# Kernel optimization log

Measured on AMD Instinct MI355X. Metric: run time of the kernel, lower is better.

## Reference

```python
import jax, jax.numpy as jnp
import numpy as np

E, D, H, K = 640000, 128, 64, 8  # edges, edge-feat dim, hidden=max(32, D//2), n_experts
TEMPERATURE = 1.0


def setup_inputs() -> dict:
    key = jax.random.key(0)
    ks = jax.random.split(key, 6)
    u = lambda k, shape, fan: jax.random.uniform(k, shape, jnp.float32, -1.0 / np.sqrt(fan), 1.0 / np.sqrt(fan))
    return {
        "edge_features": jax.random.normal(ks[0], (E, D), jnp.float32),
        "w1": u(ks[1], (D, H), D),
        "b1": u(ks[2], (H,), D),
        "w2": u(ks[3], (H, K), H),
        "b2": u(ks[4], (K,), H),
        "w_proj": u(ks[5], (D, K), D),
    }


def reference(edge_features, w1, b1, w2, b2, w_proj):
    # edge MLP router: [E, D] -> [E, H] -> [E, K]
    h = jax.nn.relu(edge_features @ w1 + b1)
    logits = (h @ w2 + b2) / TEMPERATURE
    # soft gating
    alpha = jax.nn.softmax(logits, axis=-1)  # [E, K]
    # expert scores (no bias) and weighted reduce
    expert_scores = edge_features @ w_proj   # [E, K]
    fused_edge = jnp.sum(alpha * expert_scores, axis=-1)  # [E]
    return fused_edge, alpha
```

## Files before the change

kernel.cpp:

```cpp
#include <hip/hip_runtime.h>
#include <hip/hip_bf16.h>

typedef __bf16 bf16x8 __attribute__((ext_vector_type(8)));
typedef float  f32x4  __attribute__((ext_vector_type(4)));

#define MFMA(a, b, c) __builtin_amdgcn_mfma_f32_16x16x32_bf16((a), (b), (c), 0, 0, 0)


__device__ __forceinline__ int swz(int row, int byteInRow) {
    return row * 256 + (byteInRow ^ ((row & 7) << 4));
}

__global__ __launch_bounds__(256, 3) void edge_moe_kernel(
    const float* __restrict__ x,  const float* __restrict__ w1,
    const float* __restrict__ b1, const float* __restrict__ w2,
    const float* __restrict__ b2, const float* __restrict__ wp,
    float* __restrict__ outFused, float* __restrict__ outAlpha, int E)
{
    __shared__ __align__(16) char lds[49152];
    char* XH = lds;
    char* XL = lds + 16384;
    char* HF = lds + 32768;

    const int tid  = threadIdx.x;
    const int lane = tid & 63;
    const int wid  = tid >> 6;
    const int lc   = lane & 15;
    const int lg   = lane >> 4;

    bf16x8 w1h[4], w1l[4], w2h[2], w2l[2], wph[4], wpl[4];
#pragma unroll
    for (int kk = 0; kk < 4; ++kk) {
        bf16x8 h, l;
#pragma unroll
        for (int j = 0; j < 8; ++j) {
            int kidx = kk * 32 + lg * 8 + j;
            float v = w1[kidx * 64 + wid * 16 + lc];
            __bf16 hb = (__bf16)v;
            h[j] = hb; l[j] = (__bf16)(v - (float)hb);
        }
        w1h[kk] = h; w1l[kk] = l;
    }
#pragma unroll
    for (int kk = 0; kk < 2; ++kk) {
        bf16x8 h, l;
#pragma unroll
        for (int j = 0; j < 8; ++j) {
            int kidx = kk * 32 + lg * 8 + j;
            float v = (lc < 8) ? w2[kidx * 8 + lc] : 0.0f;
            __bf16 hb = (__bf16)v;
            h[j] = hb; l[j] = (__bf16)(v - (float)hb);
        }
        w2h[kk] = h; w2l[kk] = l;
    }
#pragma unroll
    for (int kk = 0; kk < 4; ++kk) {
        bf16x8 h, l;
#pragma unroll
        for (int j = 0; j < 8; ++j) {
            int kidx = kk * 32 + lg * 8 + j;
            float v = (lc < 8) ? wp[kidx * 8 + lc] : 0.0f;
            __bf16 hb = (__bf16)v;
            h[j] = hb; l[j] = (__bf16)(v - (float)hb);
        }
        wph[kk] = h; wpl[kk] = l;
    }
    const float b1v = b1[wid * 16 + lc];
    const float b2v = (lc < 8) ? b2[lc] : 0.0f;

    const int ntiles = (E + 63) >> 6;
    const int r0 = tid >> 4;
    const int c8 = tid & 15;

    for (int tile = blockIdx.x; tile < ntiles; tile += gridDim.x) {
        const int eb = tile * 64;

        float4 vr[4][2];
#pragma unroll
        for (int it = 0; it < 4; ++it) {
            int row = r0 + it * 16;
            long long e = eb + row; if (e > (long long)E - 1) e = E - 1;
            const float4* p = (const float4*)(x + (size_t)e * 128 + c8 * 8);
            vr[it][0] = p[0];
            vr[it][1] = p[1];
        }
        __syncthreads();

#pragma unroll
        for (int it = 0; it < 4; ++it) {
            int row = r0 + it * 16;
            bf16x8 h, l;
            const float* f = (const float*)&vr[it][0];
#pragma unroll
            for (int j = 0; j < 8; ++j) {
                float v = f[j];
                __bf16 hb = (__bf16)v;
                h[j] = hb; l[j] = (__bf16)(v - (float)hb);
            }
            int off = swz(row, c8 * 16);
            *(bf16x8*)(XH + off) = h;
            *(bf16x8*)(XL + off) = l;
        }
        __syncthreads();

        f32x4 acc[4];
#pragma unroll
        for (int mt = 0; mt < 4; ++mt) {
            f32x4 a = {0.f, 0.f, 0.f, 0.f};
            int row = mt * 16 + lc;
#pragma unroll
            for (int kk = 0; kk < 4; ++kk) {
                int off = swz(row, kk * 64 + lg * 16);
                bf16x8 ah = *(const bf16x8*)(XH + off);
                bf16x8 al = *(const bf16x8*)(XL + off);
                a = MFMA(ah, w1h[kk], a);
                a = MFMA(al, w1h[kk], a);
                a = MFMA(ah, w1l[kk], a);
            }
            acc[mt] = a;
        }
#pragma unroll
        for (int mt = 0; mt < 4; ++mt) {
#pragma unroll
            for (int r = 0; r < 4; ++r) {
                float hv = fmaxf(acc[mt][r] + b1v, 0.f);
                int row = mt * 16 + lg * 4 + r;
                int col = wid * 16 + lc;
                *(float*)(HF + swz(row, col * 4)) = hv;
            }
        }
        __syncthreads();

        f32x4 lac = {0.f, 0.f, 0.f, 0.f};
        f32x4 sac = {0.f, 0.f, 0.f, 0.f};
        {
            int row = wid * 16 + lc;
#pragma unroll
            for (int kk = 0; kk < 2; ++kk) {
                int base = kk * 128 + lg * 32;
                f32x4 h0 = *(const f32x4*)(HF + swz(row, base));
                f32x4 h1 = *(const f32x4*)(HF + swz(row, base + 16));
                bf16x8 hh, hl;
#pragma unroll
                for (int j = 0; j < 4; ++j) {
                    float v0 = h0[j]; __bf16 q0 = (__bf16)v0;
                    hh[j] = q0; hl[j] = (__bf16)(v0 - (float)q0);
                    float v1 = h1[j]; __bf16 q1 = (__bf16)v1;
                    hh[j + 4] = q1; hl[j + 4] = (__bf16)(v1 - (float)q1);
                }
                lac = MFMA(hh, w2h[kk], lac);
                lac = MFMA(hl, w2h[kk], lac);
                lac = MFMA(hh, w2l[kk], lac);
            }
#pragma unroll
            for (int kk = 0; kk < 4; ++kk) {
                int off = swz(row, kk * 64 + lg * 16);
                bf16x8 ah = *(const bf16x8*)(XH + off);
                bf16x8 al = *(const bf16x8*)(XL + off);
                sac = MFMA(ah, wph[kk], sac);
                sac = MFMA(al, wph[kk], sac);
                sac = MFMA(ah, wpl[kk], sac);
            }
        }

#pragma unroll
        for (int r = 0; r < 4; ++r) {
            float lv = lac[r] + b2v;
            float m = lv;
            m = fmaxf(m, __shfl_xor(m, 1));
            m = fmaxf(m, __shfl_xor(m, 2));
            m = fmaxf(m, __shfl_xor(m, 4));
            float p = __expf(lv - m);
            float s = p;
            s += __shfl_xor(s, 1);
            s += __shfl_xor(s, 2);
            s += __shfl_xor(s, 4);
            float alpha = p / s;
            float fv = alpha * sac[r];
            fv += __shfl_xor(fv, 1);
            fv += __shfl_xor(fv, 2);
            fv += __shfl_xor(fv, 4);
            long long edge = eb + wid * 16 + lg * 4 + r;
            if (edge < E) {
                if (lc < 8) outAlpha[edge * 8 + lc] = alpha;
                if (lc == 0) outFused[edge] = fv;
            }
        }
    }
}

extern "C" void kernel_launch(void* const* d_in, const int* in_sizes, int n_in,
                              void* d_out, int out_size, void* d_ws, size_t ws_size,
                              hipStream_t stream) {
    const float* x  = (const float*)d_in[0];
    const float* w1 = (const float*)d_in[1];
    const float* b1 = (const float*)d_in[2];
    const float* w2 = (const float*)d_in[3];
    const float* b2 = (const float*)d_in[4];
    const float* wp = (const float*)d_in[5];

    const int E = in_sizes[0] / 128;
    float* outF = (float*)d_out;
    float* outA = outF + E;

    const int ntiles = (E + 63) >> 6;
    const int blocks = ntiles < 768 ? ntiles : 768;
    edge_moe_kernel<<<blocks, 256, 0, stream>>>(x, w1, b1, w2, b2, wp, outF, outA, E);
}
```

Before: 90.32 us.

## Give each wave its own edge rows, drop weight low-part MFMAs and softmax max

Each wave now computes the full hidden layer for its own 16 edges, so all four N-tiles of w1 stay in registers. The X fragments are loaded once and reused for both GEMMs, and a block-wide barrier is removed because each wave only reads its own HF rows. The low-order bf16 part of w1 and w_proj is dropped, cutting MFMA count from three passes to two. The softmax max subtraction is removed and the fused reduction shares the sum shuffles. This trades some precision and overflow safety for fewer instructions, at the cost of more weight registers.

```diff
diff --git a/kernel.cpp b/kernel.cpp
--- a/kernel.cpp
+++ b/kernel.cpp
@@ -28,19 +28,20 @@
     const int lc   = lane & 15;
     const int lg   = lane >> 4;
 
-    bf16x8 w1h[4], w1l[4], w2h[2], w2l[2], wph[4], wpl[4];
+    bf16x8 w1h[4][4];
 #pragma unroll
-    for (int kk = 0; kk < 4; ++kk) {
-        bf16x8 h, l;
+    for (int kk = 0; kk < 4; ++kk)
 #pragma unroll
-        for (int j = 0; j < 8; ++j) {
-            int kidx = kk * 32 + lg * 8 + j;
-            float v = w1[kidx * 64 + wid * 16 + lc];
-            __bf16 hb = (__bf16)v;
-            h[j] = hb; l[j] = (__bf16)(v - (float)hb);
+        for (int nt = 0; nt < 4; ++nt) {
+            bf16x8 h;
+#pragma unroll
+            for (int j = 0; j < 8; ++j) {
+                int kidx = kk * 32 + lg * 8 + j;
+                h[j] = (__bf16)w1[kidx * 64 + nt * 16 + lc];
+            }
+            w1h[kk][nt] = h;
         }
-        w1h[kk] = h; w1l[kk] = l;
-    }
+    bf16x8 w2h[2], w2l[2];
 #pragma unroll
     for (int kk = 0; kk < 2; ++kk) {
         bf16x8 h, l;
@@ -53,33 +54,35 @@
         }
         w2h[kk] = h; w2l[kk] = l;
     }
+    bf16x8 wph[4];
 #pragma unroll
     for (int kk = 0; kk < 4; ++kk) {
-        bf16x8 h, l;
+        bf16x8 h;
 #pragma unroll
         for (int j = 0; j < 8; ++j) {
             int kidx = kk * 32 + lg * 8 + j;
-            float v = (lc < 8) ? wp[kidx * 8 + lc] : 0.0f;
-            __bf16 hb = (__bf16)v;
-            h[j] = hb; l[j] = (__bf16)(v - (float)hb);
+            h[j] = (lc < 8) ? (__bf16)wp[kidx * 8 + lc] : (__bf16)0.0f;
         }
-        wph[kk] = h; wpl[kk] = l;
+        wph[kk] = h;
     }
-    const float b1v = b1[wid * 16 + lc];
+    float b1v[4];
+#pragma unroll
+    for (int nt = 0; nt < 4; ++nt) b1v[nt] = b1[nt * 16 + lc];
     const float b2v = (lc < 8) ? b2[lc] : 0.0f;
 
     const int ntiles = (E + 63) >> 6;
     const int r0 = tid >> 4;
     const int c8 = tid & 15;
+    const int arow = wid * 16 + lc;
 
     for (int tile = blockIdx.x; tile < ntiles; tile += gridDim.x) {
-        const int eb = tile * 64;
+        const long long eb = (long long)tile * 64;
 
         float4 vr[4][2];
 #pragma unroll
         for (int it = 0; it < 4; ++it) {
-            int row = r0 + it * 16;
-            long long e = eb + row; if (e > (long long)E - 1) e = E - 1;
+            long long e = eb + r0 + it * 16;
+            if (e > (long long)E - 1) e = E - 1;
             const float4* p = (const float4*)(x + (size_t)e * 128 + c8 * 8);
             vr[it][0] = p[0];
             vr[it][1] = p[1];
@@ -103,83 +106,68 @@
         }
         __syncthreads();
 
-        f32x4 acc[4];
+        bf16x8 axh[4], axl[4];
 #pragma unroll
-        for (int mt = 0; mt < 4; ++mt) {
-            f32x4 a = {0.f, 0.f, 0.f, 0.f};
-            int row = mt * 16 + lc;
+        for (int kk = 0; kk < 4; ++kk) {
+            int off = swz(arow, kk * 64 + lg * 16);
+            axh[kk] = *(const bf16x8*)(XH + off);
+            axl[kk] = *(const bf16x8*)(XL + off);
+        }
+        f32x4 acc[4] = {{0.f,0.f,0.f,0.f},{0.f,0.f,0.f,0.f},{0.f,0.f,0.f,0.f},{0.f,0.f,0.f,0.f}};
 #pragma unroll
-            for (int kk = 0; kk < 4; ++kk) {
-                int off = swz(row, kk * 64 + lg * 16);
-                bf16x8 ah = *(const bf16x8*)(XH + off);
-                bf16x8 al = *(const bf16x8*)(XL + off);
-                a = MFMA(ah, w1h[kk], a);
-                a = MFMA(al, w1h[kk], a);
-                a = MFMA(ah, w1l[kk], a);
+        for (int kk = 0; kk < 4; ++kk)
+#pragma unroll
+            for (int nt = 0; nt < 4; ++nt) {
+                acc[nt] = MFMA(axh[kk], w1h[kk][nt], acc[nt]);
+                acc[nt] = MFMA(axl[kk], w1h[kk][nt], acc[nt]);
             }
-            acc[mt] = a;
-        }
 #pragma unroll
-        for (int mt = 0; mt < 4; ++mt) {
+        for (int nt = 0; nt < 4; ++nt)
 #pragma unroll
             for (int r = 0; r < 4; ++r) {
-                float hv = fmaxf(acc[mt][r] + b1v, 0.f);
-                int row = mt * 16 + lg * 4 + r;
-                int col = wid * 16 + lc;
+                float hv = fmaxf(acc[nt][r] + b1v[nt], 0.f);
+                int row = wid * 16 + lg * 4 + r;
+                int col = nt * 16 + lc;
                 *(float*)(HF + swz(row, col * 4)) = hv;
             }
-        }
-        __syncthreads();
 
         f32x4 lac = {0.f, 0.f, 0.f, 0.f};
         f32x4 sac = {0.f, 0.f, 0.f, 0.f};
-        {
-            int row = wid * 16 + lc;
 #pragma unroll
-            for (int kk = 0; kk < 2; ++kk) {
-                int base = kk * 128 + lg * 32;
-                f32x4 h0 = *(const f32x4*)(HF + swz(row, base));
-                f32x4 h1 = *(const f32x4*)(HF + swz(row, base + 16));
-                bf16x8 hh, hl;
+        for (int kk = 0; kk < 2; ++kk) {
+            int base = kk * 128 + lg * 32;
+            f32x4 h0 = *(const f32x4*)(HF + swz(arow, base));
+            f32x4 h1 = *(const f32x4*)(HF + swz(arow, base + 16));
+            bf16x8 hh, hl;
 #pragma unroll
-                for (int j = 0; j < 4; ++j) {
-                    float v0 = h0[j]; __bf16 q0 = (__bf16)v0;
-                    hh[j] = q0; hl[j] = (__bf16)(v0 - (float)q0);
-                    float v1 = h1[j]; __bf16 q1 = (__bf16)v1;
-                    hh[j + 4] = q1; hl[j + 4] = (__bf16)(v1 - (float)q1);
-                }
-                lac = MFMA(hh, w2h[kk], lac);
-                lac = MFMA(hl, w2h[kk], lac);
-                lac = MFMA(hh, w2l[kk], lac);
+            for (int j = 0; j < 4; ++j) {
+                float v0 = h0[j]; __bf16 q0 = (__bf16)v0;
+                hh[j] = q0; hl[j] = (__bf16)(v0 - (float)q0);
+                float v1 = h1[j]; __bf16 q1 = (__bf16)v1;
+                hh[j + 4] = q1; hl[j + 4] = (__bf16)(v1 - (float)q1);
             }
+            lac = MFMA(hh, w2h[kk], lac);
+            lac = MFMA(hl, w2h[kk], lac);
+            lac = MFMA(hh, w2l[kk], lac);
+        }
 #pragma unroll
-            for (int kk = 0; kk < 4; ++kk) {
-                int off = swz(row, kk * 64 + lg * 16);
-                bf16x8 ah = *(const bf16x8*)(XH + off);
-                bf16x8 al = *(const bf16x8*)(XL + off);
-                sac = MFMA(ah, wph[kk], sac);
-                sac = MFMA(al, wph[kk], sac);
-                sac = MFMA(ah, wpl[kk], sac);
-            }
+        for (int kk = 0; kk < 4; ++kk) {
+            sac = MFMA(axh[kk], wph[kk], sac);
+            sac = MFMA(axl[kk], wph[kk], sac);
         }
 
 #pragma unroll
         for (int r = 0; r < 4; ++r) {
             float lv = lac[r] + b2v;
-            float m = lv;
-            m = fmaxf(m, __shfl_xor(m, 1));
-            m = fmaxf(m, __shfl_xor(m, 2));
-            m = fmaxf(m, __shfl_xor(m, 4));
-            float p = __expf(lv - m);
-            float s = p;
-            s += __shfl_xor(s, 1);
-            s += __shfl_xor(s, 2);
-            s += __shfl_xor(s, 4);
-            float alpha = p / s;
-            float fv = alpha * sac[r];
-            fv += __shfl_xor(fv, 1);
-            fv += __shfl_xor(fv, 2);
-            fv += __shfl_xor(fv, 4);
+            float p = __expf(lv);
+            float s  = p;
+            float fs = p * sac[r];
+            s  += __shfl_xor(s, 1);  fs += __shfl_xor(fs, 1);
+            s  += __shfl_xor(s, 2);  fs += __shfl_xor(fs, 2);
+            s  += __shfl_xor(s, 4);  fs += __shfl_xor(fs, 4);
+            float inv = 1.0f / s;
+            float alpha = p * inv;
+            float fv = fs * inv;
             long long edge = eb + wid * 16 + lg * 4 + r;
             if (edge < E) {
                 if (lc < 8) outAlpha[edge * 8 + lc] = alpha;
```

New measurement: 147.5 us. +63.3%, slower.
